# Kernel tuning notes

Hardware: AMD Instinct MI355X
Metric: run time of the kernel (lower is better)

The kernel has to match this reference:

```python
import jax, jax.numpy as jnp
import numpy as np

# ---- static geometry (matches init_kwargs) ----
B, S, D = 2, 4096, 2048
H, HD = 32, 64                      # num_heads, head_dim
HGRID, WGRID = 64, 64               # canvas h_dim, w_dim
TH, TW = 8, 16                      # tile size (th*tw = 128)
KH, KW = 16, 32                     # window (kernel) size
NTH, NTW = HGRID // TH, WGRID // TW
T = NTH * NTW                       # 32 tiles
TN = TH * TW                        # 128 tokens per tile
KTH, KTW = KH // TH, KW // TW
K = KTH * KTW                       # 4 kv tiles per query tile
SCALE = 1.0 / np.sqrt(HD)


def _kv_tile_ids():
    # For each query tile, the K kv tiles inside its (clamped) sliding window.
    qt = np.arange(T)
    qh, qw = qt // NTW, qt % NTW
    lbh, rbh = KTH // 2, KTH // 2 + (KTH % 2 - 1)
    lbw, rbw = KTW // 2, KTW // 2 + (KTW % 2 - 1)
    ch = np.clip(qh, lbh, NTH - 1 - rbh)
    cw = np.clip(qw, lbw, NTW - 1 - rbw)
    hh = ch[:, None] - lbh + np.arange(KTH)          # [T, KTH]
    ww = cw[:, None] - lbw + np.arange(KTW)          # [T, KTW]
    return (hh[:, :, None] * NTW + ww[:, None, :]).reshape(T, K)

KV_TILES = jnp.asarray(_kv_tile_ids())  # [T, K] int


def _to_tiles(x):
    # [B, S, H, HD] (row-major h,w) -> [B, H, T, TN, HD] (tile-major)
    x = x.reshape(B, NTH, TH, NTW, TW, H, HD)
    x = x.transpose(0, 5, 1, 3, 2, 4, 6)  # B,H,nth,ntw,th,tw,hd
    return x.reshape(B, H, T, TN, HD)


def _from_tiles(x):
    # [B, H, T, TN, HD] -> [B, S, H*HD]
    x = x.reshape(B, H, NTH, NTW, TH, TW, HD)
    x = x.transpose(0, 2, 4, 3, 5, 1, 6)  # B,nth,th,ntw,tw,H,hd
    return x.reshape(B, S, H * HD)


def setup_inputs() -> dict:
    key = jax.random.key(0)
    ks = jax.random.split(key, 5)
    sw = 1.0 / np.sqrt(D)
    return {
        "hidden_states": jax.random.normal(ks[0], (B, S, D), jnp.float32),
        "Wq": jax.random.normal(ks[1], (D, D), jnp.float32) * sw,
        "Wk": jax.random.normal(ks[2], (D, D), jnp.float32) * sw,
        "Wv": jax.random.normal(ks[3], (D, D), jnp.float32) * sw,
        "Wo": jax.random.normal(ks[4], (D, D), jnp.float32) * sw,
    }


def reference(hidden_states, Wq, Wk, Wv, Wo):
    # projections (weights stored [in, out]; equivalent to nn.Linear math)
    q = _to_tiles((hidden_states @ Wq).reshape(B, S, H, HD))  # [B,H,T,TN,HD]
    k = _to_tiles((hidden_states @ Wk).reshape(B, S, H, HD))
    v = _to_tiles((hidden_states @ Wv).reshape(B, S, H, HD))

    # gather the K allowed kv tiles for every query tile (block-sparse pattern)
    kg = k[:, :, KV_TILES].reshape(B, H, T, K * TN, HD)  # [B,H,T,K*TN,HD]
    vg = v[:, :, KV_TILES].reshape(B, H, T, K * TN, HD)

    # dense attention within each block (all gathered tokens are valid)
    scores = jnp.einsum("bhtqd,bhtkd->bhtqk", q, kg) * SCALE
    attn = jax.nn.softmax(scores, axis=-1)
    o = jnp.einsum("bhtqk,bhtkd->bhtqd", attn, vg)  # [B,H,T,TN,HD]

    return _from_tiles(o) @ Wo  # [B, S, D]
```

## Files before the change

kernel.cpp:

```cpp
#include <hip/hip_runtime.h>

typedef __bf16 bf16;
typedef __attribute__((ext_vector_type(8))) __bf16 bf16x8;
typedef __attribute__((ext_vector_type(4))) __bf16 bf16x4;
typedef __attribute__((ext_vector_type(4))) float f32x4;

#define MFMA16(a, b, c) __builtin_amdgcn_mfma_f32_16x16x32_bf16((a), (b), (c), 0, 0, 0)

__device__ __forceinline__ void gload16(const void* g, void* lds) {
  __builtin_amdgcn_global_load_lds(
      (__attribute__((address_space(1))) unsigned int*)(unsigned long long)g,
      (__attribute__((address_space(3))) unsigned int*)lds, 16, 0, 0);
}

__global__ void __launch_bounds__(256) cast_x_kernel(const float* __restrict__ X,
                                                     bf16* __restrict__ Xb) {
  int i = (blockIdx.x * 256 + threadIdx.x) * 4;
  f32x4 v = *(const f32x4*)(X + i);
  bf16x4 o;
  o[0] = (bf16)v[0]; o[1] = (bf16)v[1]; o[2] = (bf16)v[2]; o[3] = (bf16)v[3];
  *(bf16x4*)(Xb + i) = o;
}

__global__ void __launch_bounds__(256) transpose_w3_kernel(const float* __restrict__ Wq,
                                                           const float* __restrict__ Wk,
                                                           const float* __restrict__ Wv,
                                                           bf16* __restrict__ T0,
                                                           bf16* __restrict__ T1,
                                                           bf16* __restrict__ T2) {
  __shared__ float tile[64][65];
  int which = blockIdx.x >> 10;
  int bid = blockIdx.x & 1023;
  const float* W = which == 0 ? Wq : (which == 1 ? Wk : Wv);
  bf16* WT = which == 0 ? T0 : (which == 1 ? T1 : T2);
  int n0 = (bid & 31) * 64;
  int k0 = (bid >> 5) * 64;
  int tid = threadIdx.x;
  int r = tid >> 4;
  int c4 = (tid & 15) * 4;
#pragma unroll
  for (int i = 0; i < 4; ++i) {
    f32x4 v = *(const f32x4*)(W + (size_t)(k0 + r + i * 16) * 2048 + n0 + c4);
    tile[r + i * 16][c4 + 0] = v[0];
    tile[r + i * 16][c4 + 1] = v[1];
    tile[r + i * 16][c4 + 2] = v[2];
    tile[r + i * 16][c4 + 3] = v[3];
  }
  __syncthreads();
#pragma unroll
  for (int i = 0; i < 4; ++i) {
    int n = r + i * 16;
    bf16x4 o;
    o[0] = (bf16)tile[c4 + 0][n];
    o[1] = (bf16)tile[c4 + 1][n];
    o[2] = (bf16)tile[c4 + 2][n];
    o[3] = (bf16)tile[c4 + 3][n];
    *(bf16x4*)(WT + (size_t)(n0 + n) * 2048 + k0 + c4) = o;
  }
}

__global__ void __launch_bounds__(256) transpose_w_kernel(const float* __restrict__ W,
                                                          bf16* __restrict__ WT) {
  __shared__ float tile[64][65];
  int n0 = (blockIdx.x & 31) * 64;
  int k0 = (blockIdx.x >> 5) * 64;
  int tid = threadIdx.x;
  int r = tid >> 4;
  int c4 = (tid & 15) * 4;
#pragma unroll
  for (int i = 0; i < 4; ++i) {
    f32x4 v = *(const f32x4*)(W + (size_t)(k0 + r + i * 16) * 2048 + n0 + c4);
    tile[r + i * 16][c4 + 0] = v[0];
    tile[r + i * 16][c4 + 1] = v[1];
    tile[r + i * 16][c4 + 2] = v[2];
    tile[r + i * 16][c4 + 3] = v[3];
  }
  __syncthreads();
#pragma unroll
  for (int i = 0; i < 4; ++i) {
    int n = r + i * 16;
    bf16x4 o;
    o[0] = (bf16)tile[c4 + 0][n];
    o[1] = (bf16)tile[c4 + 1][n];
    o[2] = (bf16)tile[c4 + 2][n];
    o[3] = (bf16)tile[c4 + 3][n];
    *(bf16x4*)(WT + (size_t)(n0 + n) * 2048 + k0 + c4) = o;
  }
}

__device__ __forceinline__ void gemm256_core(const bf16* __restrict__ Ag,
                                             const bf16* __restrict__ Bg,
                                             char* lds, f32x4 (&acc)[8][4]) {
  const int tid = threadIdx.x;
  const int lane = tid & 63, wid = tid >> 6;
  const int g = lane >> 4, r16 = lane & 15;
  const int wm = wid >> 2, wn = wid & 3;
  const int swz = ((g ^ ((r16 >> 1) & 3)) << 4);

  const int srow = wid * 32 + (lane >> 2);
  const int scol = ((lane & 3) ^ ((lane >> 3) & 3)) * 8;
  const bf16* gA = Ag + (size_t)srow * 2048 + scol;
  const bf16* gB = Bg + (size_t)srow * 2048 + scol;
  char* sA = lds + wid * 2048;
  char* sB = lds + 16384 + wid * 2048;

  const int arow0 = wm * 128 + r16;
  const int brow0 = wn * 64 + r16;

#define STAGE_A(bf_, tt_)                              \
  {                                                    \
    char* d_ = sA + (bf_) * 32768;                     \
    const bf16* s_ = gA + (size_t)(tt_) * 32;          \
    gload16(s_, d_);                                   \
    gload16(s_ + (size_t)16 * 2048, d_ + 1024);        \
  }
#define STAGE_B(bf_, tt_)                              \
  {                                                    \
    char* d_ = sB + (bf_) * 32768;                     \
    const bf16* s_ = gB + (size_t)(tt_) * 32;          \
    gload16(s_, d_);                                   \
    gload16(s_ + (size_t)16 * 2048, d_ + 1024);        \
  }

  STAGE_A(0, 0) STAGE_B(0, 0) STAGE_A(1, 1) STAGE_B(1, 1)
  asm volatile("s_waitcnt vmcnt(4)" ::: "memory");
  __builtin_amdgcn_s_barrier();
  __builtin_amdgcn_sched_barrier(0);

  int c = 0;
  for (int t = 0; t < 64; ++t) {
    const char* Ab = lds + c * 32768;
    const char* Bb = Ab + 16384;
    int sbuf = c + 2; if (sbuf >= 3) sbuf -= 3;

    bf16x8 bfr[4], af[8];
#pragma unroll
    for (int j = 0; j < 4; ++j)
      bfr[j] = *(const bf16x8*)(Bb + (brow0 + j * 16) * 64 + swz);
#pragma unroll
    for (int i = 0; i < 8; ++i)
      af[i] = *(const bf16x8*)(Ab + (arow0 + i * 16) * 64 + swz);

    if (t < 62) { STAGE_A(sbuf, t + 2) STAGE_B(sbuf, t + 2) }

#pragma unroll
    for (int i = 0; i < 8; ++i)
#pragma unroll
      for (int j = 0; j < 4; ++j)
        acc[i][j] = MFMA16(af[i], bfr[j], acc[i][j]);

    if (t < 62) {
      asm volatile("s_waitcnt vmcnt(4)" ::: "memory");
    } else if (t == 62) {
      asm volatile("s_waitcnt vmcnt(0)" ::: "memory");
    }
    __builtin_amdgcn_s_barrier();
    __builtin_amdgcn_sched_barrier(0);

    c += 1; if (c >= 3) c -= 3;
  }
#undef STAGE_A
#undef STAGE_B
}

__global__ void __launch_bounds__(512, 2) gemm_qkv_kernel(
    const bf16* __restrict__ Xb, const bf16* __restrict__ W0, const bf16* __restrict__ W1,
    const bf16* __restrict__ W2, bf16* __restrict__ q_t, bf16* __restrict__ k_t,
    bf16* __restrict__ v_t) {
  __shared__ char lds[98304];
  int bid = blockIdx.x;
  int xcd = bid & 7, idx = bid >> 3;
  int by = xcd * 4 + idx / 24, bx = idx % 24;
  int which = bx >> 3;
  int m0 = by * 256, n0 = (bx & 7) * 256;
  const bf16* W = which == 0 ? W0 : (which == 1 ? W1 : W2);

  f32x4 acc[8][4] = {};
  gemm256_core(Xb + (size_t)m0 * 2048, W + (size_t)n0 * 2048, lds, acc);

  int lane = threadIdx.x & 63, wid = threadIdx.x >> 6;
  int g = lane >> 4, r16 = lane & 15;
  int wm = wid >> 2, wn = wid & 3;
#pragma unroll
  for (int i = 0; i < 8; ++i) {
#pragma unroll
    for (int r = 0; r < 4; ++r) {
      int m = m0 + wm * 128 + i * 16 + g * 4 + r;
      int b = m >> 12, s = m & 4095;
      int hg = s >> 6, wg = s & 63;
      int t = ((hg >> 3) << 2) + (wg >> 4);
      int tn = ((hg & 7) << 4) + (wg & 15);
#pragma unroll
      for (int j = 0; j < 4; ++j) {
        int n = n0 + wn * 64 + j * 16 + r16;
        int h = n >> 6, hd = n & 63;
        float val = acc[i][j][r];
        size_t base = ((size_t)(b * 32 + h) * 32 + t);
        if (which == 0)
          q_t[(base * 128 + tn) * 64 + hd] = (bf16)(val * 0.125f);
        else if (which == 1)
          k_t[(base * 128 + tn) * 64 + hd] = (bf16)val;
        else
          v_t[(base * 64 + hd) * 128 + tn] = (bf16)val;
      }
    }
  }
}

__global__ void __launch_bounds__(512, 2) gemm_out_kernel(const bf16* __restrict__ A,
                                                          const bf16* __restrict__ W,
                                                          float* __restrict__ C) {
  __shared__ char lds[98304];
  int bid = blockIdx.x;
  int xcd = bid & 7, idx = bid >> 3;
  int by = xcd * 4 + idx / 8, bx = idx & 7;
  int m0 = by * 256, n0 = bx * 256;

  f32x4 acc[8][4] = {};
  gemm256_core(A + (size_t)m0 * 2048, W + (size_t)n0 * 2048, lds, acc);

  int lane = threadIdx.x & 63, wid = threadIdx.x >> 6;
  int g = lane >> 4, r16 = lane & 15;
  int wm = wid >> 2, wn = wid & 3;
#pragma unroll
  for (int i = 0; i < 8; ++i)
#pragma unroll
    for (int j = 0; j < 4; ++j)
#pragma unroll
      for (int r = 0; r < 4; ++r) {
        int m = m0 + wm * 128 + i * 16 + g * 4 + r;
        int n = n0 + wn * 64 + j * 16 + r16;
        C[(size_t)m * 2048 + n] = acc[i][j][r];
      }
}

__global__ void __launch_bounds__(256) attn_kernel(const bf16* __restrict__ q_t,
                                                   const bf16* __restrict__ k_t,
                                                   const bf16* __restrict__ v_t,
                                                   bf16* __restrict__ o_bf) {
  __shared__ char Pl[128 * 256];
  int bid = blockIdx.x;
  int bh = (bid & 7) * 8 + (bid >> 8);
  int t = (bid >> 3) & 31;
  int h = bh & 31, b = bh >> 5;
  int tid = threadIdx.x, w = tid >> 6, lane = tid & 63;
  int g = lane >> 4, r16 = lane & 15;

  const size_t qoff = ((size_t)bh * 32 + t) * (128 * 64);
  bf16x8 qf[2][2];
#pragma unroll
  for (int mf = 0; mf < 2; ++mf)
#pragma unroll
    for (int kf = 0; kf < 2; ++kf)
      qf[mf][kf] = *(const bf16x8*)&q_t[qoff + (size_t)(w * 32 + mf * 16 + r16) * 64 + kf * 32 + g * 8];

  f32x4 oacc[2][4] = {};
  float mrun[2][4], lrun[2][4];
#pragma unroll
  for (int mf = 0; mf < 2; ++mf)
#pragma unroll
    for (int r = 0; r < 4; ++r) { mrun[mf][r] = -1e30f; lrun[mf][r] = 0.f; }

  int qh = t >> 2, qw = t & 3;
  int ch = qh < 1 ? 1 : (qh > 7 ? 7 : qh);
  int cw = qw < 1 ? 1 : (qw > 3 ? 3 : qw);

  for (int c = 0; c < 4; ++c) {
    int vt = (ch - 1 + (c >> 1)) * 4 + (cw - 1 + (c & 1));
    const bf16* Kt = k_t + ((size_t)bh * 32 + vt) * (128 * 64);
    const bf16* Vt = v_t + ((size_t)bh * 32 + vt) * (128 * 64);

    f32x4 s[2][8];
#pragma unroll
    for (int nf = 0; nf < 8; ++nf) {
      bf16x8 kf0 = *(const bf16x8*)&Kt[(nf * 16 + r16) * 64 + g * 8];
      bf16x8 kf1 = *(const bf16x8*)&Kt[(nf * 16 + r16) * 64 + 32 + g * 8];
#pragma unroll
      for (int mf = 0; mf < 2; ++mf) {
        f32x4 z = {};
        z = MFMA16(qf[mf][0], kf0, z);
        z = MFMA16(qf[mf][1], kf1, z);
        s[mf][nf] = z;
      }
    }

#pragma unroll
    for (int mf = 0; mf < 2; ++mf) {
#pragma unroll
      for (int r = 0; r < 4; ++r) {
        float mx = s[mf][0][r];
#pragma unroll
        for (int nf = 1; nf < 8; ++nf) mx = fmaxf(mx, s[mf][nf][r]);
        mx = fmaxf(mx, __shfl_xor(mx, 1));
        mx = fmaxf(mx, __shfl_xor(mx, 2));
        mx = fmaxf(mx, __shfl_xor(mx, 4));
        mx = fmaxf(mx, __shfl_xor(mx, 8));
        float mold = mrun[mf][r];
        float mnew = fmaxf(mold, mx);
        float sc = __expf(mold - mnew);
        mrun[mf][r] = mnew;
        float ps = 0.f;
#pragma unroll
        for (int nf = 0; nf < 8; ++nf) {
          float p = __expf(s[mf][nf][r] - mnew);
          s[mf][nf][r] = p;
          ps += p;
        }
        ps += __shfl_xor(ps, 1);
        ps += __shfl_xor(ps, 2);
        ps += __shfl_xor(ps, 4);
        ps += __shfl_xor(ps, 8);
        lrun[mf][r] = lrun[mf][r] * sc + ps;
#pragma unroll
        for (int hf = 0; hf < 4; ++hf) oacc[mf][hf][r] *= sc;
      }
    }

#pragma unroll
    for (int mf = 0; mf < 2; ++mf)
#pragma unroll
      for (int r = 0; r < 4; ++r) {
        int row = w * 32 + mf * 16 + g * 4 + r;
        int rb = row * 256;
        int swzp = (row & 7) << 4;
#pragma unroll
        for (int nf = 0; nf < 8; ++nf) {
          int addr = (rb + (nf * 16 + r16) * 2) ^ swzp;
          *(bf16*)(Pl + addr) = (bf16)s[mf][nf][r];
        }
      }
    __syncthreads();

#pragma unroll
    for (int ks = 0; ks < 4; ++ks) {
      bf16x8 pf[2];
#pragma unroll
      for (int mf = 0; mf < 2; ++mf) {
        int row = w * 32 + mf * 16 + r16;
        int addr = (row * 256 + ks * 64 + g * 16) ^ ((row & 7) << 4);
        pf[mf] = *(const bf16x8*)(Pl + addr);
      }
      bf16x8 vf[4];
#pragma unroll
      for (int hf = 0; hf < 4; ++hf)
        vf[hf] = *(const bf16x8*)&Vt[(hf * 16 + r16) * 128 + ks * 32 + g * 8];
#pragma unroll
      for (int mf = 0; mf < 2; ++mf)
#pragma unroll
        for (int hf = 0; hf < 4; ++hf)
          oacc[mf][hf] = MFMA16(pf[mf], vf[hf], oacc[mf][hf]);
    }
    __syncthreads();
  }

  int nth = t >> 2, ntw = t & 3;
#pragma unroll
  for (int mf = 0; mf < 2; ++mf)
#pragma unroll
    for (int r = 0; r < 4; ++r) {
      float inv = __builtin_amdgcn_rcpf(lrun[mf][r]);
      int tn = w * 32 + mf * 16 + g * 4 + r;
      int stok = (nth * 8 + (tn >> 4)) * 64 + ntw * 16 + (tn & 15);
#pragma unroll
      for (int hf = 0; hf < 4; ++hf) {
        int col = h * 64 + hf * 16 + r16;
        o_bf[((size_t)b * 4096 + stok) * 2048 + col] = (bf16)(oacc[mf][hf][r] * inv);
      }
    }
}

extern "C" void kernel_launch(void* const* d_in, const int* in_sizes, int n_in,
                              void* d_out, int out_size, void* d_ws, size_t ws_size,
                              hipStream_t stream) {
  const float* X = (const float*)d_in[0];
  const float* Wq = (const float*)d_in[1];
  const float* Wk = (const float*)d_in[2];
  const float* Wv = (const float*)d_in[3];
  const float* Wo = (const float*)d_in[4];
  float* out = (float*)d_out;
  char* ws = (char*)d_ws;
  if (ws_size < 159383552u) return;

  bf16* Xb  = (bf16*)(ws + 0);
  bf16* WT0 = (bf16*)(ws + 33554432u);
  bf16* WT1 = (bf16*)(ws + 41943040u);
  bf16* WT2 = (bf16*)(ws + 50331648u);
  bf16* q_t = (bf16*)(ws + 58720256u);
  bf16* k_t = (bf16*)(ws + 92274688u);
  bf16* v_t = (bf16*)(ws + 125829120u);
  bf16* o_bf = Xb;

  cast_x_kernel<<<16384, 256, 0, stream>>>(X, Xb);
  transpose_w3_kernel<<<3072, 256, 0, stream>>>(Wq, Wk, Wv, WT0, WT1, WT2);
  gemm_qkv_kernel<<<768, 512, 0, stream>>>(Xb, WT0, WT1, WT2, q_t, k_t, v_t);
  attn_kernel<<<2048, 256, 0, stream>>>(q_t, k_t, v_t, o_bf);
  transpose_w_kernel<<<1024, 256, 0, stream>>>(Wo, WT0);
  gemm_out_kernel<<<256, 512, 0, stream>>>(o_bf, WT0, out);
}
```

Measured before the change: 504.6 us.

## Shrink GEMM tiles to 128x128 with 256-thread blocks and MFMA priority

Replaces the 256x256 tile, 512-thread GEMM core with a 128x128 tile, 256-thread core for both the QKV and output projections. This quadruples the block count and halves LDS per block, aimed at better CU occupancy and load balance (the output GEMM previously had only 256 blocks). It also raises wave priority around the MFMA loop via s_setprio. The cost is lower per-block data reuse, so more global and L2 traffic per FLOP.

```diff
diff --git a/kernel.cpp b/kernel.cpp
--- a/kernel.cpp
+++ b/kernel.cpp
@@ -88,66 +88,64 @@
   }
 }
 
-__device__ __forceinline__ void gemm256_core(const bf16* __restrict__ Ag,
+__device__ __forceinline__ void gemm128_core(const bf16* __restrict__ Ag,
                                              const bf16* __restrict__ Bg,
-                                             char* lds, f32x4 (&acc)[8][4]) {
+                                             char* lds, f32x4 (&acc)[4][4]) {
   const int tid = threadIdx.x;
   const int lane = tid & 63, wid = tid >> 6;
   const int g = lane >> 4, r16 = lane & 15;
-  const int wm = wid >> 2, wn = wid & 3;
+  const int wm = wid >> 1, wn = wid & 1;
   const int swz = ((g ^ ((r16 >> 1) & 3)) << 4);
 
-  const int srow = wid * 32 + (lane >> 2);
+  const int srow = wid * 16 + (lane >> 2);
   const int scol = ((lane & 3) ^ ((lane >> 3) & 3)) * 8;
   const bf16* gA = Ag + (size_t)srow * 2048 + scol;
   const bf16* gB = Bg + (size_t)srow * 2048 + scol;
-  char* sA = lds + wid * 2048;
-  char* sB = lds + 16384 + wid * 2048;
-
-  const int arow0 = wm * 128 + r16;
+  char* dst0 = lds + tid * 16;
+
+  const int arow0 = wm * 64 + r16;
   const int brow0 = wn * 64 + r16;
 
-#define STAGE_A(bf_, tt_)                              \
+#define STAGE(bf_, tt_)                                \
   {                                                    \
-    char* d_ = sA + (bf_) * 32768;                     \
-    const bf16* s_ = gA + (size_t)(tt_) * 32;          \
-    gload16(s_, d_);                                   \
-    gload16(s_ + (size_t)16 * 2048, d_ + 1024);        \
-  }
-#define STAGE_B(bf_, tt_)                              \
-  {                                                    \
-    char* d_ = sB + (bf_) * 32768;                     \
-    const bf16* s_ = gB + (size_t)(tt_) * 32;          \
-    gload16(s_, d_);                                   \
-    gload16(s_ + (size_t)16 * 2048, d_ + 1024);        \
-  }
-
-  STAGE_A(0, 0) STAGE_B(0, 0) STAGE_A(1, 1) STAGE_B(1, 1)
+    char* dA_ = dst0 + (bf_) * 16384;                  \
+    const bf16* sA_ = gA + (size_t)(tt_) * 32;         \
+    gload16(sA_, dA_);                                 \
+    gload16(sA_ + (size_t)64 * 2048, dA_ + 4096);      \
+    char* dB_ = dA_ + 8192;                            \
+    const bf16* sB_ = gB + (size_t)(tt_) * 32;         \
+    gload16(sB_, dB_);                                 \
+    gload16(sB_ + (size_t)64 * 2048, dB_ + 4096);      \
+  }
+
+  STAGE(0, 0) STAGE(1, 1)
   asm volatile("s_waitcnt vmcnt(4)" ::: "memory");
   __builtin_amdgcn_s_barrier();
   __builtin_amdgcn_sched_barrier(0);
 
   int c = 0;
   for (int t = 0; t < 64; ++t) {
-    const char* Ab = lds + c * 32768;
-    const char* Bb = Ab + 16384;
+    const char* Ab = lds + c * 16384;
+    const char* Bb = Ab + 8192;
     int sbuf = c + 2; if (sbuf >= 3) sbuf -= 3;
 
-    bf16x8 bfr[4], af[8];
+    bf16x8 af[4], bfr[4];
 #pragma unroll
     for (int j = 0; j < 4; ++j)
       bfr[j] = *(const bf16x8*)(Bb + (brow0 + j * 16) * 64 + swz);
 #pragma unroll
-    for (int i = 0; i < 8; ++i)
+    for (int i = 0; i < 4; ++i)
       af[i] = *(const bf16x8*)(Ab + (arow0 + i * 16) * 64 + swz);
 
-    if (t < 62) { STAGE_A(sbuf, t + 2) STAGE_B(sbuf, t + 2) }
-
-#pragma unroll
-    for (int i = 0; i < 8; ++i)
+    if (t < 62) STAGE(sbuf, t + 2)
+
+    __builtin_amdgcn_s_setprio(1);
+#pragma unroll
+    for (int i = 0; i < 4; ++i)
 #pragma unroll
       for (int j = 0; j < 4; ++j)
         acc[i][j] = MFMA16(af[i], bfr[j], acc[i][j]);
+    __builtin_amdgcn_s_setprio(0);
 
     if (t < 62) {
       asm volatile("s_waitcnt vmcnt(4)" ::: "memory");
@@ -159,33 +157,32 @@
 
     c += 1; if (c >= 3) c -= 3;
   }
-#undef STAGE_A
-#undef STAGE_B
-}
-
-__global__ void __launch_bounds__(512, 2) gemm_qkv_kernel(
+#undef STAGE
+}
+
+__global__ void __launch_bounds__(256) gemm_qkv_kernel(
     const bf16* __restrict__ Xb, const bf16* __restrict__ W0, const bf16* __restrict__ W1,
     const bf16* __restrict__ W2, bf16* __restrict__ q_t, bf16* __restrict__ k_t,
     bf16* __restrict__ v_t) {
-  __shared__ char lds[98304];
+  __shared__ char lds[49152];
   int bid = blockIdx.x;
   int xcd = bid & 7, idx = bid >> 3;
-  int by = xcd * 4 + idx / 24, bx = idx % 24;
-  int which = bx >> 3;
-  int m0 = by * 256, n0 = (bx & 7) * 256;
+  int dm = idx & 7, ncol = idx >> 3;
+  int which = ncol >> 4;
+  int m0 = (xcd * 8 + dm) * 128, n0 = (ncol & 15) * 128;
   const bf16* W = which == 0 ? W0 : (which == 1 ? W1 : W2);
 
-  f32x4 acc[8][4] = {};
-  gemm256_core(Xb + (size_t)m0 * 2048, W + (size_t)n0 * 2048, lds, acc);
+  f32x4 acc[4][4] = {};
+  gemm128_core(Xb + (size_t)m0 * 2048, W + (size_t)n0 * 2048, lds, acc);
 
   int lane = threadIdx.x & 63, wid = threadIdx.x >> 6;
   int g = lane >> 4, r16 = lane & 15;
-  int wm = wid >> 2, wn = wid & 3;
-#pragma unroll
-  for (int i = 0; i < 8; ++i) {
+  int wm = wid >> 1, wn = wid & 1;
+#pragma unroll
+  for (int i = 0; i < 4; ++i) {
 #pragma unroll
     for (int r = 0; r < 4; ++r) {
-      int m = m0 + wm * 128 + i * 16 + g * 4 + r;
+      int m = m0 + wm * 64 + i * 16 + g * 4 + r;
       int b = m >> 12, s = m & 4095;
       int hg = s >> 6, wg = s & 63;
       int t = ((hg >> 3) << 2) + (wg >> 4);
@@ -207,28 +204,28 @@
   }
 }
 
-__global__ void __launch_bounds__(512, 2) gemm_out_kernel(const bf16* __restrict__ A,
-                                                          const bf16* __restrict__ W,
-                                                          float* __restrict__ C) {
-  __shared__ char lds[98304];
+__global__ void __launch_bounds__(256) gemm_out_kernel(const bf16* __restrict__ A,
+                                                       const bf16* __restrict__ W,
+                                                       float* __restrict__ C) {
+  __shared__ char lds[49152];
   int bid = blockIdx.x;
   int xcd = bid & 7, idx = bid >> 3;
-  int by = xcd * 4 + idx / 8, bx = idx & 7;
-  int m0 = by * 256, n0 = bx * 256;
-
-  f32x4 acc[8][4] = {};
-  gemm256_core(A + (size_t)m0 * 2048, W + (size_t)n0 * 2048, lds, acc);
+  int dm = idx & 7, nn = idx >> 3;
+  int m0 = (xcd * 8 + dm) * 128, n0 = nn * 128;
+
+  f32x4 acc[4][4] = {};
+  gemm128_core(A + (size_t)m0 * 2048, W + (size_t)n0 * 2048, lds, acc);
 
   int lane = threadIdx.x & 63, wid = threadIdx.x >> 6;
   int g = lane >> 4, r16 = lane & 15;
-  int wm = wid >> 2, wn = wid & 3;
-#pragma unroll
-  for (int i = 0; i < 8; ++i)
+  int wm = wid >> 1, wn = wid & 1;
+#pragma unroll
+  for (int i = 0; i < 4; ++i)
 #pragma unroll
     for (int j = 0; j < 4; ++j)
 #pragma unroll
       for (int r = 0; r < 4; ++r) {
-        int m = m0 + wm * 128 + i * 16 + g * 4 + r;
+        int m = m0 + wm * 64 + i * 16 + g * 4 + r;
         int n = n0 + wn * 64 + j * 16 + r16;
         C[(size_t)m * 2048 + n] = acc[i][j][r];
       }
@@ -392,8 +389,8 @@
 
   cast_x_kernel<<<16384, 256, 0, stream>>>(X, Xb);
   transpose_w3_kernel<<<3072, 256, 0, stream>>>(Wq, Wk, Wv, WT0, WT1, WT2);
-  gemm_qkv_kernel<<<768, 512, 0, stream>>>(Xb, WT0, WT1, WT2, q_t, k_t, v_t);
+  gemm_qkv_kernel<<<3072, 256, 0, stream>>>(Xb, WT0, WT1, WT2, q_t, k_t, v_t);
   attn_kernel<<<2048, 256, 0, stream>>>(q_t, k_t, v_t, o_bf);
   transpose_w_kernel<<<1024, 256, 0, stream>>>(Wo, WT0);
-  gemm_out_kernel<<<256, 512, 0, stream>>>(o_bf, WT0, out);
-}
+  gemm_out_kernel<<<1024, 256, 0, stream>>>(o_bf, WT0, out);
+}
```

New measurement: 546.4 us. +8.3%, slower.
